# Kernel tuning notes

Hardware: AMD Instinct MI355X
Metric: run time of the kernel (lower is better)

The kernel has to match this reference:

```python
import jax, jax.numpy as jnp
import numpy as np

D_MODEL = 1024
N_HEADS = 16
D_KEYS = D_MODEL // N_HEADS


def setup_inputs() -> dict:
    key = jax.random.key(0)
    ks = jax.random.split(key, 11)
    B, L, S = 2, 2048, 2048
    inp = {
        "queries": jax.random.normal(ks[0], (B, L, D_MODEL), dtype=jnp.float32),
        "keys": jax.random.normal(ks[1], (B, S, D_MODEL), dtype=jnp.float32),
        "values": jax.random.normal(ks[2], (B, S, D_MODEL), dtype=jnp.float32),
        # Linear params, scaled like torch default init (~U(-1/sqrt(D), 1/sqrt(D)))
        "Wq": jax.random.normal(ks[3], (D_MODEL, D_MODEL), dtype=jnp.float32) / np.sqrt(D_MODEL),
        "bq": jax.random.normal(ks[4], (D_MODEL,), dtype=jnp.float32) / np.sqrt(D_MODEL),
        "Wk": jax.random.normal(ks[5], (D_MODEL, D_MODEL), dtype=jnp.float32) / np.sqrt(D_MODEL),
        "bk": jax.random.normal(ks[6], (D_MODEL,), dtype=jnp.float32) / np.sqrt(D_MODEL),
        "Wv": jax.random.normal(ks[7], (D_MODEL, D_MODEL), dtype=jnp.float32) / np.sqrt(D_MODEL),
        "bv": jax.random.normal(ks[8], (D_MODEL,), dtype=jnp.float32) / np.sqrt(D_MODEL),
        "Wo": jax.random.normal(ks[9], (D_MODEL, D_MODEL), dtype=jnp.float32) / np.sqrt(D_MODEL),
        "bo": jax.random.normal(ks[10], (D_MODEL,), dtype=jnp.float32) / np.sqrt(D_MODEL),
    }
    return inp


def reference(queries, keys, values, Wq, bq, Wk, bk, Wv, bv, Wo, bo):
    B, L, _ = queries.shape
    S = keys.shape[1]
    H, E = N_HEADS, D_KEYS
    scale = E ** (-0.5)
    q = (queries @ Wq.T + bq).reshape(B, L, H, E)
    k = (keys @ Wk.T + bk).reshape(B, S, H, E)
    v = (values @ Wv.T + bv).reshape(B, S, H, E)
    scores = jnp.einsum('blhe,bshe->bhls', q, k)
    attn = jax.nn.softmax(scores * scale, axis=-1)  # dropout = identity in eval
    out = jnp.einsum('bhls,bshe->blhe', attn, v).reshape(B, L, H * E)
    return out @ Wo.T + bo
```

## Files before the change

kernel.cpp:

```cpp
#include <hip/hip_runtime.h>

typedef unsigned short u16;
typedef unsigned int u32;
typedef __attribute__((ext_vector_type(8))) short short8;
typedef __attribute__((ext_vector_type(4))) short s16x4;
typedef __attribute__((ext_vector_type(4))) float f32x4;
typedef __attribute__((ext_vector_type(16))) float f32x16;

#define DEVI __device__ __forceinline__

#define LSEQ 2048
#define DMODEL 1024
#define NH 16
#define EHD 64

#define QSCALE 0.18033688011112042f

#if __has_builtin(__builtin_amdgcn_exp2f)
#define EXP2(x) __builtin_amdgcn_exp2f(x)
#else
#define EXP2(x) exp2f(x)
#endif

DEVI u16 f2b(float f) {
    u32 u = __float_as_uint(f);
    return (u16)((u + 0x7FFFu + ((u >> 16) & 1u)) >> 16);
}

DEVI u32 cvtpk(float lo, float hi) {
    u32 r;
    asm("v_cvt_pk_bf16_f32 %0, %1, %2" : "=v"(r) : "v"(lo), "v"(hi));
    return r;
}

DEVI void swap32(u32& a, u32& b) {
    asm("v_permlane32_swap_b32 %0, %1" : "+v"(a), "+v"(b));
}

DEVI short8 mk8(u32 a0, u32 a1, u32 a2, u32 a3) {
    union { u32 u[4]; short8 s; } x;
    x.u[0] = a0; x.u[1] = a1; x.u[2] = a2; x.u[3] = a3;
    return x.s;
}

DEVI void async_cp16(const void* g, void* l) {
    __builtin_amdgcn_global_load_lds((const __attribute__((address_space(1))) u32*)g,
                                     (__attribute__((address_space(3))) u32*)l, 16, 0, 0);
}

DEVI short8 lds_swz(const u16* base, int row, int colb) {
    int off = (row << 7) + (colb ^ ((row & 7) << 4));
    return *(const short8*)((const char*)base + off);
}

__global__ __launch_bounds__(256) void cvt_all(const float* __restrict__ q,
                                               const float* __restrict__ k,
                                               const float* __restrict__ v,
                                               const float* __restrict__ wq,
                                               const float* __restrict__ wk,
                                               const float* __restrict__ wv,
                                               const float* __restrict__ wo,
                                               u16* __restrict__ dst) {
    const size_t NX8 = (size_t)2 * LSEQ * DMODEL / 8;
    const size_t NW8 = (size_t)DMODEL * DMODEL / 8;
    int bid = blockIdx.x;
    const float* src;
    size_t base;
    int rel;
    if (bid < 2048)      { src = q;  base = 0;             rel = bid; }
    else if (bid < 4096) { src = k;  base = NX8;           rel = bid - 2048; }
    else if (bid < 6144) { src = v;  base = 2 * NX8;       rel = bid - 4096; }
    else if (bid < 6656) { src = wq; base = 3 * NX8;             rel = bid - 6144; }
    else if (bid < 7168) { src = wk; base = 3 * NX8 + NW8;       rel = bid - 6656; }
    else if (bid < 7680) { src = wv; base = 3 * NX8 + 2 * NW8;   rel = bid - 7168; }
    else                 { src = wo; base = 3 * NX8 + 3 * NW8;   rel = bid - 7680; }
    size_t i = (size_t)rel * 256 + threadIdx.x;
    const float4* p = (const float4*)(src + i * 8);
    float4 a = p[0], c = p[1];
    short8 o;
    o[0] = (short)f2b(a.x); o[1] = (short)f2b(a.y);
    o[2] = (short)f2b(a.z); o[3] = (short)f2b(a.w);
    o[4] = (short)f2b(c.x); o[5] = (short)f2b(c.y);
    o[6] = (short)f2b(c.z); o[7] = (short)f2b(c.w);
    *(short8*)(dst + (base + i) * 8) = o;
}

__global__ __launch_bounds__(256, 5) void gemm_qkv(const u16* __restrict__ X,
                                                   const u16* __restrict__ W3,
                                                   const float* __restrict__ bq,
                                                   const float* __restrict__ bk,
                                                   const float* __restrict__ bv,
                                                   u16* __restrict__ Qp,
                                                   u16* __restrict__ Kp,
                                                   u16* __restrict__ Vt) {
    __shared__ __align__(16) u16 As[2][4096];
    __shared__ __align__(16) u16 Bs[2][2048];
    const int tid = threadIdx.x;
    const int lane = tid & 63, w = tid >> 6;
    const int lr = lane & 15, lk = lane >> 4;
    const int wr = w >> 1, wc = w & 1;
    const int bid = blockIdx.x;
    const int xcd = bid & 7, rr = bid >> 3;
    const int rb = (xcd * 4 + rr / 48) * 128;
    const int xtile = rr % 48;
    const int cb = xtile * 64;
    const int K = DMODEL;
    const int seg = xtile >> 4;
    const u16* A = X + (size_t)seg * ((size_t)2 * LSEQ * DMODEL);

    f32x4 acc[4][2] = {};

    const int sra = tid >> 2, ska = (tid & 3) * 8;

#define QKV_STAGE(bb, kk)                                                            \
    do {                                                                             \
        async_cp16(A + (size_t)(rb + sra) * K + (kk) + ska, &As[bb][tid * 8]);       \
        async_cp16(A + (size_t)(rb + 64 + sra) * K + (kk) + ska,                     \
                   &As[bb][2048 + tid * 8]);                                         \
        async_cp16(W3 + (size_t)(cb + sra) * K + (kk) + ska, &Bs[bb][tid * 8]);      \
    } while (0)

    QKV_STAGE(0, 0);
    asm volatile("s_waitcnt vmcnt(0)" ::: "memory");
    __syncthreads();

    int cur = 0;
    for (int k0 = 0; k0 < K; k0 += 32) {
        if (k0 + 32 < K) QKV_STAGE(cur ^ 1, k0 + 32);

        short8 af[4], bfr[2];
#pragma unroll
        for (int m = 0; m < 4; m++)
            af[m] = *(const short8*)(&As[cur][(wr * 64 + m * 16 + lr) * 32 + lk * 8]);
#pragma unroll
        for (int n = 0; n < 2; n++)
            bfr[n] = *(const short8*)(&Bs[cur][(wc * 32 + n * 16 + lr) * 32 + lk * 8]);
        __builtin_amdgcn_s_setprio(1);
#pragma unroll
        for (int m = 0; m < 4; m++)
#pragma unroll
            for (int n = 0; n < 2; n++)
                acc[m][n] = __builtin_amdgcn_mfma_f32_16x16x32_bf16(af[m], bfr[n], acc[m][n], 0, 0, 0);
        __builtin_amdgcn_s_setprio(0);

        asm volatile("s_waitcnt vmcnt(0)" ::: "memory");
        __syncthreads();
        cur ^= 1;
    }

    const float* bp = seg == 0 ? bq : (seg == 1 ? bk : bv);
    const float sc = seg == 0 ? QSCALE : 1.0f;

#pragma unroll
    for (int n = 0; n < 2; n++) {
        int col = cb + wc * 32 + n * 16 + lr;
        int c2 = col & 1023;
        float bvv = bp[c2];
#pragma unroll
        for (int m = 0; m < 4; m++) {
            int row0 = rb + wr * 64 + m * 16 + lk * 4;
            if (seg == 2) {
                s16x4 pk4;
#pragma unroll
                for (int r = 0; r < 4; r++) pk4[r] = (short)f2b(acc[m][n][r] + bvv);
                size_t idx = (((size_t)(row0 >> 11) * NH + (c2 >> 6)) * EHD + (c2 & 63)) * LSEQ +
                             (row0 & (LSEQ - 1));
                *(s16x4*)(Vt + idx) = pk4;
            } else {
                u16* dst = seg == 0 ? Qp : Kp;
#pragma unroll
                for (int r = 0; r < 4; r++)
                    dst[(size_t)(row0 + r) * DMODEL + c2] = f2b((acc[m][n][r] + bvv) * sc);
            }
        }
    }
}

__global__ __launch_bounds__(256) void gemm_out(const u16* __restrict__ A,
                                                const u16* __restrict__ B,
                                                const float* __restrict__ bias,
                                                float* __restrict__ C) {
    __shared__ __align__(16) u16 As[3][4096];
    __shared__ __align__(16) u16 Bs[3][2048];
    const int tid = threadIdx.x;
    const int lane = tid & 63, w = tid >> 6;
    const int lr = lane & 15, lk = lane >> 4;
    const int wr = w >> 1, wc = w & 1;
    const int bid = blockIdx.x;
    const int xcd = bid & 7, rr = bid >> 3;
    const int rb = (xcd * 4 + rr / 16) * 128;
    const int cb = (rr % 16) * 64;
    const int K = DMODEL, N = DMODEL;

    f32x4 acc[4][2] = {};

    const int arow = lane >> 2;
    const int acol = (lane & 3) * 8;

#define OUT_STAGE(bb, kk)                                                           \
    do {                                                                            \
        _Pragma("unroll") for (int c2 = 0; c2 < 2; ++c2) {                          \
            int c = w * 2 + c2;                                                     \
            async_cp16(A + (size_t)(rb + c * 16 + arow) * K + (kk) + acol,          \
                       &As[bb][c * 512]);                                           \
        }                                                                           \
        async_cp16(B + (size_t)(cb + w * 16 + arow) * K + (kk) + acol,              \
                   &Bs[bb][w * 512]);                                               \
    } while (0)

#define OUT_ITER(bc, bs, tt)                                                          \
    do {                                                                              \
        if ((tt) + 2 < 32) OUT_STAGE(bs, ((tt) + 2) * 32);                            \
        short8 af[4], bfr[2];                                                         \
        _Pragma("unroll") for (int m = 0; m < 4; m++)                                 \
            af[m] = *(const short8*)(&As[bc][(wr * 64 + m * 16 + lr) * 32 + lk * 8]); \
        _Pragma("unroll") for (int n = 0; n < 2; n++)                                 \
            bfr[n] = *(const short8*)(&Bs[bc][(wc * 32 + n * 16 + lr) * 32 + lk * 8]); \
        __builtin_amdgcn_s_setprio(1);                                                \
        _Pragma("unroll") for (int m = 0; m < 4; m++)                                 \
            _Pragma("unroll") for (int n = 0; n < 2; n++)                             \
                acc[m][n] =                                                           \
                    __builtin_amdgcn_mfma_f32_16x16x32_bf16(af[m], bfr[n], acc[m][n], 0, 0, 0); \
        __builtin_amdgcn_s_setprio(0);                                                \
        if ((tt) + 2 < 32) asm volatile("s_waitcnt vmcnt(3)" ::: "memory");           \
        else               asm volatile("s_waitcnt vmcnt(0)" ::: "memory");           \
        __builtin_amdgcn_s_barrier();                                                 \
    } while (0)

    OUT_STAGE(0, 0);
    OUT_STAGE(1, 32);
    asm volatile("s_waitcnt vmcnt(3)" ::: "memory");
    __builtin_amdgcn_s_barrier();

    for (int tb = 0; tb < 30; tb += 3) {
        OUT_ITER(0, 2, tb);
        OUT_ITER(1, 0, tb + 1);
        OUT_ITER(2, 1, tb + 2);
    }
    OUT_ITER(0, 2, 30);
    OUT_ITER(1, 0, 31);

#pragma unroll
    for (int n = 0; n < 2; n++) {
        int col = cb + wc * 32 + n * 16 + lr;
        float bv = bias[col];
#pragma unroll
        for (int m = 0; m < 4; m++) {
            int row0 = rb + wr * 64 + m * 16 + lk * 4;
#pragma unroll
            for (int r = 0; r < 4; r++)
                C[(size_t)(row0 + r) * N + col] = acc[m][n][r] + bv;
        }
    }
}

__global__ __launch_bounds__(512) void attn_kernel(const u16* __restrict__ Q,
                                                   const u16* __restrict__ Kp,
                                                   const u16* __restrict__ Vtb,
                                                   u16* __restrict__ Hid) {
    const int bid = blockIdx.x;
    const int j = bid >> 3;
    const int bh = (bid & 7) + 8 * (j >> 3);
    const int q0 = (j & 7) * 256;
    const int b = bh >> 4, h = bh & 15;
    const int tid = threadIdx.x, lane = tid & 63, w = tid >> 6;
    const int l31 = lane & 31, hi = lane >> 5;
    const int qb = q0 + w * 32;

    __shared__ __align__(16) u16 Ks[2][8192];
    __shared__ __align__(16) u16 Vs[2][2][4096];

    short8 qf[4];
#pragma unroll
    for (int eg = 0; eg < 4; eg++)
        qf[eg] = *(const short8*)(Q + (size_t)(b * LSEQ + qb + l31) * DMODEL + h * EHD +
                                  eg * 16 + hi * 8);

    const int trow = tid >> 3;
    const int slot = tid & 7;
    const int swz8 = ((slot ^ (trow & 7)) * 8);
    size_t kbase[2], vbase[2];
#pragma unroll
    for (int jj = 0; jj < 2; jj++) {
        kbase[jj] = (size_t)(b * LSEQ + jj * 64 + trow) * DMODEL + h * EHD + swz8;
        vbase[jj] = ((size_t)bh * EHD + trow) * LSEQ + jj * 64 + swz8;
    }

#define ATTN_STAGE(bb, s0v)                                                           \
    do {                                                                              \
        async_cp16(Kp + kbase[0] + (size_t)(s0v)*DMODEL, &Ks[bb][w * 512]);           \
        async_cp16(Kp + kbase[1] + (size_t)(s0v)*DMODEL, &Ks[bb][4096 + w * 512]);    \
        async_cp16(Vtb + vbase[0] + (s0v), &Vs[bb][0][w * 512]);                      \
        async_cp16(Vtb + vbase[1] + (s0v), &Vs[bb][1][w * 512]);                      \
    } while (0)

    f32x16 o0 = (f32x16)0.f, o1 = (f32x16)0.f, lsum = (f32x16)0.f;
    const u32 one2 = 0x3F803F80u;
    const short8 ones = mk8(one2, one2, one2, one2);

    ATTN_STAGE(0, 0);
    asm volatile("s_waitcnt vmcnt(0)" ::: "memory");
    __syncthreads();

    int cur = 0;
    for (int t = 0; t < LSEQ / 128; ++t) {
        if (t + 1 < LSEQ / 128) ATTN_STAGE(cur ^ 1, (t + 1) * 128);

#pragma unroll
        for (int hf = 0; hf < 2; hf++) {
            f32x16 s0 = (f32x16)0.f, s1 = (f32x16)0.f;
            __builtin_amdgcn_s_setprio(1);
#pragma unroll
            for (int eg = 0; eg < 4; eg++) {
                short8 kf0 = lds_swz(&Ks[cur][0], hf * 64 + l31, eg * 32 + hi * 16);
                short8 kf1 = lds_swz(&Ks[cur][0], hf * 64 + 32 + l31, eg * 32 + hi * 16);
                s0 = __builtin_amdgcn_mfma_f32_32x32x16_bf16(kf0, qf[eg], s0, 0, 0, 0);
                s1 = __builtin_amdgcn_mfma_f32_32x32x16_bf16(kf1, qf[eg], s1, 0, 0, 0);
            }
            __builtin_amdgcn_s_setprio(0);

#pragma unroll
            for (int r = 0; r < 16; r++) {
                s0[r] = EXP2(s0[r]);
                s1[r] = EXP2(s1[r]);
            }

            short8 paf[4];
#pragma unroll
            for (int kc = 0; kc < 4; kc++) {
                int ro = (kc & 1) * 8;
                u32 u0, u1, u2, u3;
                if (kc < 2) {
                    u0 = cvtpk(s0[ro + 0], s0[ro + 1]); u1 = cvtpk(s0[ro + 2], s0[ro + 3]);
                    u2 = cvtpk(s0[ro + 4], s0[ro + 5]); u3 = cvtpk(s0[ro + 6], s0[ro + 7]);
                } else {
                    u0 = cvtpk(s1[ro + 0], s1[ro + 1]); u1 = cvtpk(s1[ro + 2], s1[ro + 3]);
                    u2 = cvtpk(s1[ro + 4], s1[ro + 5]); u3 = cvtpk(s1[ro + 6], s1[ro + 7]);
                }
                swap32(u0, u2);
                swap32(u1, u3);
                paf[kc] = mk8(u0, u1, u2, u3);
            }

            __builtin_amdgcn_s_setprio(1);
#pragma unroll
            for (int kc = 0; kc < 4; kc++) {
                short8 vf0 = lds_swz(&Vs[cur][hf][0], l31, kc * 32 + hi * 16);
                short8 vf1 = lds_swz(&Vs[cur][hf][0], 32 + l31, kc * 32 + hi * 16);
                o0 = __builtin_amdgcn_mfma_f32_32x32x16_bf16(paf[kc], vf0, o0, 0, 0, 0);
                o1 = __builtin_amdgcn_mfma_f32_32x32x16_bf16(paf[kc], vf1, o1, 0, 0, 0);
                lsum = __builtin_amdgcn_mfma_f32_32x32x16_bf16(paf[kc], ones, lsum, 0, 0, 0);
            }
            __builtin_amdgcn_s_setprio(0);
        }

        asm volatile("s_waitcnt vmcnt(0)" ::: "memory");
        __syncthreads();
        cur ^= 1;
    }

#pragma unroll
    for (int r = 0; r < 16; r++) {
        float li = 1.0f / lsum[r];
        int qrow = qb + (r & 3) + 8 * (r >> 2) + 4 * hi;
        size_t base = (size_t)(b * LSEQ + qrow) * DMODEL + h * EHD;
        Hid[base + l31] = f2b(o0[r] * li);
        Hid[base + 32 + l31] = f2b(o1[r] * li);
    }
}

extern "C" void kernel_launch(void* const* d_in, const int* in_sizes, int n_in,
                              void* d_out, int out_size, void* d_ws, size_t ws_size,
                              hipStream_t stream) {
    const float* queries = (const float*)d_in[0];
    const float* keys    = (const float*)d_in[1];
    const float* values  = (const float*)d_in[2];
    const float* Wq = (const float*)d_in[3];
    const float* bq = (const float*)d_in[4];
    const float* Wk = (const float*)d_in[5];
    const float* bk = (const float*)d_in[6];
    const float* Wv = (const float*)d_in[7];
    const float* bv = (const float*)d_in[8];
    const float* Wo = (const float*)d_in[9];
    const float* bo = (const float*)d_in[10];
    float* out = (float*)d_out;

    const size_t NX = (size_t)2 * LSEQ * DMODEL;
    const size_t NW = (size_t)DMODEL * DMODEL;

    u16* p = (u16*)d_ws;
    u16* Xq = p;  p += NX;
    u16* Xk = p;  p += NX;
    u16* Xv = p;  p += NX;
    u16* Wqb = p; p += NW;
    u16* Wkb = p; p += NW;
    u16* Wvb = p; p += NW;
    u16* Wob = p; p += NW;
    u16* Qp = p;  p += NX;
    u16* Kp = p;  p += NX;
    u16* Vt = p;  p += NX;
    u16* Hid = p; p += NX;
    (void)Xk; (void)Xv; (void)Wkb; (void)Wvb;

    cvt_all<<<8192, 256, 0, stream>>>(queries, keys, values, Wq, Wk, Wv, Wo, Xq);

    gemm_qkv<<<1536, 256, 0, stream>>>(Xq, Wqb, bq, bk, bv, Qp, Kp, Vt);

    attn_kernel<<<256, 512, 0, stream>>>(Qp, Kp, Vt, Hid);

    gemm_out<<<512, 256, 0, stream>>>(Hid, Wob, bo, out);
}
```

Measured before the change: 131.6 us.

## Retile QKV projection GEMM to 256x256 tiles with swizzled LDS

Measured after the change: 117.6 us. -10.6%, faster.

```diff
diff --git a/kernel.cpp b/kernel.cpp
--- a/kernel.cpp
+++ b/kernel.cpp
@@ -85,7 +85,7 @@
     *(short8*)(dst + (base + i) * 8) = o;
 }
 
-__global__ __launch_bounds__(256, 5) void gemm_qkv(const u16* __restrict__ X,
+__global__ __launch_bounds__(512, 1) void gemm_qkv(const u16* __restrict__ X,
                                                    const u16* __restrict__ W3,
                                                    const float* __restrict__ bq,
                                                    const float* __restrict__ bk,
@@ -93,58 +93,88 @@
                                                    u16* __restrict__ Qp,
                                                    u16* __restrict__ Kp,
                                                    u16* __restrict__ Vt) {
-    __shared__ __align__(16) u16 As[2][4096];
-    __shared__ __align__(16) u16 Bs[2][2048];
+    __shared__ __align__(16) u16 As[2][16384];
+    __shared__ __align__(16) u16 Bs[2][16384];
     const int tid = threadIdx.x;
-    const int lane = tid & 63, w = tid >> 6;
+    const int lane = tid & 63;
+    const int w = tid >> 6;
     const int lr = lane & 15, lk = lane >> 4;
-    const int wr = w >> 1, wc = w & 1;
+    const int wm = w >> 2, wn = w & 3;
     const int bid = blockIdx.x;
     const int xcd = bid & 7, rr = bid >> 3;
-    const int rb = (xcd * 4 + rr / 48) * 128;
-    const int xtile = rr % 48;
-    const int cb = xtile * 64;
+    const int rb = (xcd * 2 + rr / 12) * 256;
+    const int cb = (rr % 12) * 256;
     const int K = DMODEL;
-    const int seg = xtile >> 4;
+    const int seg = cb >> 10;
     const u16* A = X + (size_t)seg * ((size_t)2 * LSEQ * DMODEL);
 
-    f32x4 acc[4][2] = {};
-
-    const int sra = tid >> 2, ska = (tid & 3) * 8;
-
-#define QKV_STAGE(bb, kk)                                                            \
-    do {                                                                             \
-        async_cp16(A + (size_t)(rb + sra) * K + (kk) + ska, &As[bb][tid * 8]);       \
-        async_cp16(A + (size_t)(rb + 64 + sra) * K + (kk) + ska,                     \
-                   &As[bb][2048 + tid * 8]);                                         \
-        async_cp16(W3 + (size_t)(cb + sra) * K + (kk) + ska, &Bs[bb][tid * 8]);      \
-    } while (0)
-
-    QKV_STAGE(0, 0);
+    f32x4 acc[8][4] = {};
+
+    const int srow = tid >> 3;
+    const int sslot = tid & 7;
+    size_t abase[4], bbase[4];
+#pragma unroll
+    for (int i = 0; i < 4; i++) {
+        int row = i * 64 + srow;
+        int swz = ((sslot ^ (row & 7)) * 8);
+        abase[i] = (size_t)(rb + row) * K + swz;
+        bbase[i] = (size_t)(cb + row) * K + swz;
+    }
+
+#define QS_A(bb, kk)                                                         \
+    do {                                                                     \
+        _Pragma("unroll") for (int i = 0; i < 4; i++)                        \
+            async_cp16(A + abase[i] + (kk), &As[bb][(i * 512 + tid) * 8]);   \
+    } while (0)
+#define QS_B(bb, kk)                                                         \
+    do {                                                                     \
+        _Pragma("unroll") for (int i = 0; i < 4; i++)                        \
+            async_cp16(W3 + bbase[i] + (kk), &Bs[bb][(i * 512 + tid) * 8]);  \
+    } while (0)
+
+#define QKV_MM(ac_, mt)                                                                   \
+    do {                                                                                  \
+        short8 a0 = lds_swz(ac_, wm * 128 + (mt) * 16 + lr, lk * 16);                     \
+        short8 a1 = lds_swz(ac_, wm * 128 + (mt) * 16 + lr, 64 + lk * 16);                \
+        short8 a2 = lds_swz(ac_, wm * 128 + (mt) * 16 + 16 + lr, lk * 16);                \
+        short8 a3 = lds_swz(ac_, wm * 128 + (mt) * 16 + 16 + lr, 64 + lk * 16);           \
+        __builtin_amdgcn_s_setprio(1);                                                    \
+        _Pragma("unroll") for (int n = 0; n < 4; n++) {                                   \
+            acc[mt][n] = __builtin_amdgcn_mfma_f32_16x16x32_bf16(a0, bf[n][0], acc[mt][n], 0, 0, 0);       \
+            acc[mt][n] = __builtin_amdgcn_mfma_f32_16x16x32_bf16(a1, bf[n][1], acc[mt][n], 0, 0, 0);       \
+            acc[(mt) + 1][n] = __builtin_amdgcn_mfma_f32_16x16x32_bf16(a2, bf[n][0], acc[(mt) + 1][n], 0, 0, 0); \
+            acc[(mt) + 1][n] = __builtin_amdgcn_mfma_f32_16x16x32_bf16(a3, bf[n][1], acc[(mt) + 1][n], 0, 0, 0); \
+        }                                                                                 \
+        __builtin_amdgcn_s_setprio(0);                                                    \
+    } while (0)
+
+    QS_A(0, 0);
+    QS_B(0, 0);
     asm volatile("s_waitcnt vmcnt(0)" ::: "memory");
-    __syncthreads();
+    __builtin_amdgcn_s_barrier();
 
     int cur = 0;
-    for (int k0 = 0; k0 < K; k0 += 32) {
-        if (k0 + 32 < K) QKV_STAGE(cur ^ 1, k0 + 32);
-
-        short8 af[4], bfr[2];
-#pragma unroll
-        for (int m = 0; m < 4; m++)
-            af[m] = *(const short8*)(&As[cur][(wr * 64 + m * 16 + lr) * 32 + lk * 8]);
-#pragma unroll
-        for (int n = 0; n < 2; n++)
-            bfr[n] = *(const short8*)(&Bs[cur][(wc * 32 + n * 16 + lr) * 32 + lk * 8]);
-        __builtin_amdgcn_s_setprio(1);
-#pragma unroll
-        for (int m = 0; m < 4; m++)
-#pragma unroll
-            for (int n = 0; n < 2; n++)
-                acc[m][n] = __builtin_amdgcn_mfma_f32_16x16x32_bf16(af[m], bfr[n], acc[m][n], 0, 0, 0);
-        __builtin_amdgcn_s_setprio(0);
+    for (int t = 0; t < 16; ++t) {
+        const u16* ac = &As[cur][0];
+        const u16* bc = &Bs[cur][0];
+        const bool st = (t + 1 < 16);
+        const int kk = (t + 1) * 64;
+
+        if (st) QS_A(cur ^ 1, kk);
+        short8 bf[4][2];
+#pragma unroll
+        for (int n = 0; n < 4; n++) {
+            bf[n][0] = lds_swz(bc, wn * 64 + n * 16 + lr, lk * 16);
+            bf[n][1] = lds_swz(bc, wn * 64 + n * 16 + lr, 64 + lk * 16);
+        }
+        QKV_MM(ac, 0);
+        if (st) QS_B(cur ^ 1, kk);
+        QKV_MM(ac, 2);
+        QKV_MM(ac, 4);
+        QKV_MM(ac, 6);
 
         asm volatile("s_waitcnt vmcnt(0)" ::: "memory");
-        __syncthreads();
+        __builtin_amdgcn_s_barrier();
         cur ^= 1;
     }
 
@@ -152,13 +182,13 @@
     const float sc = seg == 0 ? QSCALE : 1.0f;
 
 #pragma unroll
-    for (int n = 0; n < 2; n++) {
-        int col = cb + wc * 32 + n * 16 + lr;
+    for (int n = 0; n < 4; n++) {
+        int col = cb + wn * 64 + n * 16 + lr;
         int c2 = col & 1023;
         float bvv = bp[c2];
 #pragma unroll
-        for (int m = 0; m < 4; m++) {
-            int row0 = rb + wr * 64 + m * 16 + lk * 4;
+        for (int m = 0; m < 8; m++) {
+            int row0 = rb + wm * 128 + m * 16 + lk * 4;
             if (seg == 2) {
                 s16x4 pk4;
 #pragma unroll
@@ -404,7 +434,7 @@
 
     cvt_all<<<8192, 256, 0, stream>>>(queries, keys, values, Wq, Wk, Wv, Wo, Xq);
 
-    gemm_qkv<<<1536, 256, 0, stream>>>(Xq, Wqb, bq, bk, bv, Qp, Kp, Vt);
+    gemm_qkv<<<192, 512, 0, stream>>>(Xq, Wqb, bq, bk, bv, Qp, Kp, Vt);
 
     attn_kernel<<<256, 512, 0, stream>>>(Qp, Kp, Vt, Hid);
 
```
